# Kernel tuning notes

Measured on AMD Instinct MI355X. Metric: run time of the kernel, lower is better.

The kernel has to match this reference:

```python
import jax, jax.numpy as jnp
import numpy as np

B, T, IN, H, L, P = 512, 512, 1, 100, 4, 0.5  # batch, seq, input, hidden, layers, dropout


def setup_inputs() -> dict:
    key = jax.random.key(0)
    ks = jax.random.split(key, 12)
    k = 1.0 / np.sqrt(H)  # torch nn.LSTM init scale
    u = lambda kk, shape: jax.random.uniform(kk, shape, jnp.float32, -k, k)
    inp = {
        "x": jax.random.normal(ks[0], (B, T, IN), jnp.float32),
        "W_ih0": u(ks[1], (4 * H, IN)),          # layer 0 input weights
        "W_ih_rest": u(ks[2], (L - 1, 4 * H, H)),  # layers 1..3 input weights
        "W_hh": u(ks[3], (L, 4 * H, H)),
        "b_ih": u(ks[4], (L, 4 * H)),
        "b_hh": u(ks[5], (L, 4 * H)),
        "W_out": u(ks[6], (1, H)),
        "b_out": u(ks[7], (1,)),
        # inter-layer dropout keep-masks (torch applies dropout to outputs of layers 0..L-2)
        "drop_masks": jax.random.bernoulli(ks[8], 1.0 - P, (L - 1, B, T, H)).astype(jnp.float32),
    }
    return inp


def _lstm_layer(seq, Wih, Whh, b):
    # seq: [T, B, in_dim]; returns [T, B, H]. PyTorch gate order: i, f, g, o.
    h0 = jnp.zeros((seq.shape[1], Whh.shape[-1]), seq.dtype)

    def step(carry, xt):
        h, c = carry
        gates = xt @ Wih.T + h @ Whh.T + b  # [B, 4H]
        i, f, g, o = jnp.split(gates, 4, axis=-1)
        c = jax.nn.sigmoid(f) * c + jax.nn.sigmoid(i) * jnp.tanh(g)
        h = jax.nn.sigmoid(o) * jnp.tanh(c)
        return (h, c), h

    _, hs = jax.lax.scan(step, (h0, h0), seq)
    return hs


def reference(x, W_ih0, W_ih_rest, W_hh, b_ih, b_hh, W_out, b_out, drop_masks):
    scale = 1.0 / (1.0 - P)
    seq = jnp.swapaxes(x, 0, 1)  # [T, B, IN] (batch_first -> time-major)
    seq = _lstm_layer(seq, W_ih0, W_hh[0], b_ih[0] + b_hh[0])
    for l in range(1, L):
        seq = seq * (jnp.swapaxes(drop_masks[l - 1], 0, 1) * scale)
        seq = _lstm_layer(seq, W_ih_rest[l - 1], W_hh[l], b_ih[l] + b_hh[l])
    last = seq[-1]  # [B, H] == lstm_out[:, -1]
    return last @ W_out.T + b_out  # [B, 1]
```

## Files before the change

kernel.cpp:

```cpp
#include <hip/hip_runtime.h>
#include <cstdint>
#include <cstddef>

#define BB 512
#define TT 512
#define HH 100
#define G4 400

template<bool IS_L0, bool WRITE_DROP>
__global__ __launch_bounds__(448, 1)
void rec_kernel(const float* __restrict__ x,
                const float* __restrict__ xc,
                const float* __restrict__ Whh_l,
                const float* __restrict__ Wih0,
                const float* __restrict__ bih_l,
                const float* __restrict__ bhh_l,
                const float* __restrict__ dmask_l,
                float* __restrict__ hdrop,
                float* __restrict__ st_h,
                float* __restrict__ st_c)
{
    __shared__ float sh[G4 * HH];

    const int tid  = threadIdx.x;
    const int e    = (tid < 224) ? 0 : 1;
    const int off  = tid - e * 224;
    const int j    = off >> 1;
    const int role = off & 1;
    const bool active = (j < HH);
    const int jc   = active ? j : (HH - 1);
    const int r0   = role * 100 + jc;
    const int r1   = r0 + 200;
    const int b    = blockIdx.x * 2 + e;

    {
        const float4* src = (const float4*)Whh_l;
        float4* dst = (float4*)sh;
        for (int i = tid; i < G4 * HH / 4; i += 448) dst[i] = src[i];
    }
    __syncthreads();

    float4 wf0[25], wf1[25];
    {
        const float4* s0 = (const float4*)&sh[r0 * HH];
        const float4* s1 = (const float4*)&sh[r1 * HH];
        #pragma unroll
        for (int m = 0; m < 25; ++m) { wf0[m] = s0[m]; wf1[m] = s1[m]; }
    }
    __syncthreads();

    for (int i = tid; i < G4 * HH; i += 448) sh[i] = 0.f;

    float wx0 = 0.f, wx1 = 0.f, bs0 = 0.f, bs1 = 0.f;
    if (IS_L0) {
        wx0 = Wih0[r0];  bs0 = bih_l[r0] + bhh_l[r0];
        wx1 = Wih0[r1];  bs1 = bih_l[r1] + bhh_l[r1];
    }

    const bool isB = (role == 1);
    float c2 = 0.f, hlast = 0.f;

    __syncthreads();

    float gin0 = 0.f, gin1 = 0.f, xv = 0.f, mk = 0.f;
    if (IS_L0) {
        xv = x[(size_t)b * TT];
    } else {
        gin0 = xc[(size_t)b * G4 + r0];
        gin1 = xc[(size_t)b * G4 + r1];
    }
    if (WRITE_DROP && isB && active) mk = dmask_l[(size_t)b * TT * HH + jc];

    int cur = 0;
    for (int t = 0; t < TT; ++t) {
        const int tn = (t + 1 < TT) ? (t + 1) : t;

        float nxv = 0.f, ngin0 = 0.f, ngin1 = 0.f, nmk = 0.f;
        if (IS_L0) {
            nxv = x[(size_t)b * TT + tn];
        } else {
            const size_t base = (size_t)tn * (BB * G4) + (size_t)b * G4;
            ngin0 = xc[base + r0];
            ngin1 = xc[base + r1];
        }
        if (WRITE_DROP && isB && active)
            nmk = dmask_l[((size_t)b * TT + tn) * HH + jc];

        if (IS_L0) {
            gin0 = fmaf(xv, wx0, bs0);
            gin1 = fmaf(xv, wx1, bs1);
        }

        float a0 = 0.f, a0b = 0.f, a1 = 0.f, a1b = 0.f;
        {
            const float4* hp = (const float4*)&sh[cur * 224 + e * 112];
            #pragma unroll
            for (int m = 0; m < 25; ++m) {
                const float4 hv = hp[m];
                a0  = fmaf(wf0[m].x, hv.x, a0);
                a0b = fmaf(wf0[m].y, hv.y, a0b);
                a0  = fmaf(wf0[m].z, hv.z, a0);
                a0b = fmaf(wf0[m].w, hv.w, a0b);
                a1  = fmaf(wf1[m].x, hv.x, a1);
                a1b = fmaf(wf1[m].y, hv.y, a1b);
                a1  = fmaf(wf1[m].z, hv.z, a1);
                a1b = fmaf(wf1[m].w, hv.w, a1b);
            }
        }
        const float pre0 = a0 + a0b + gin0;
        const float pre1 = a1 + a1b + gin1;

        const float s0 = 1.f / (1.f + __expf(-pre0));
        const float E1 = __expf(isB ? (-pre1) : (pre1 + pre1));
        const float rr = 1.f / (1.f + E1);
        const float s1 = isB ? rr : fmaf(-2.f, rr, 1.f);

        const float pv   = s0 * s1;
        const float recv = __shfl_xor(pv, 1);

        const int nxt = cur ^ 1;
        if (isB) {
            c2 = fmaf(s0, c2, recv);
            const float Ec = __expf(c2 + c2);
            const float th = 1.f - 2.f / (Ec + 1.f);
            const float h  = s1 * th;
            hlast = h;
            if (active) {
                sh[nxt * 224 + e * 112 + j] = h;
                if (WRITE_DROP)
                    hdrop[((size_t)t * BB + b) * HH + j] = h * mk * 2.f;
            }
        }
        __syncthreads();
        cur = nxt;
        gin0 = ngin0; gin1 = ngin1; xv = nxv; mk = nmk;
    }

    if (isB && active) {
        st_h[(size_t)b * HH + j] = hlast;
        st_c[(size_t)b * HH + j] = c2;
    }
}

__global__ __launch_bounds__(256, 2)
void xc_gemm(const float* __restrict__ A,
             const float* __restrict__ W,
             const float* __restrict__ bih_l,
             const float* __restrict__ bhh_l,
             float* __restrict__ xc)
{
    __shared__ float At[HH][132];
    __shared__ float Bt[HH][68];

    const int tid = threadIdx.x;
    const int n0  = blockIdx.x * 64;
    const size_t m0 = (size_t)blockIdx.y * 128;

    for (int s = tid; s < 128 * 25; s += 256) {
        const int r = s / 25, kq = s - r * 25;
        const float4 v = *(const float4*)&A[(m0 + r) * HH + kq * 4];
        At[kq * 4 + 0][r] = v.x; At[kq * 4 + 1][r] = v.y;
        At[kq * 4 + 2][r] = v.z; At[kq * 4 + 3][r] = v.w;
    }
    for (int s = tid; s < 64 * 25; s += 256) {
        const int r = s / 25, kq = s - r * 25;
        const int col = n0 + r;
        float4 v = {0.f, 0.f, 0.f, 0.f};
        if (col < G4) v = *(const float4*)&W[(size_t)col * HH + kq * 4];
        Bt[kq * 4 + 0][r] = v.x; Bt[kq * 4 + 1][r] = v.y;
        Bt[kq * 4 + 2][r] = v.z; Bt[kq * 4 + 3][r] = v.w;
    }
    __syncthreads();

    const int tx = tid & 15;
    const int ty = tid >> 4;
    float acc[8][4];
    #pragma unroll
    for (int i = 0; i < 8; ++i)
        #pragma unroll
        for (int j = 0; j < 4; ++j) acc[i][j] = 0.f;

    #pragma unroll 4
    for (int k = 0; k < HH; ++k) {
        const float4 a0 = *(const float4*)&At[k][ty * 8];
        const float4 a1 = *(const float4*)&At[k][ty * 8 + 4];
        const float4 bv = *(const float4*)&Bt[k][tx * 4];
        const float av[8] = {a0.x, a0.y, a0.z, a0.w, a1.x, a1.y, a1.z, a1.w};
        #pragma unroll
        for (int i = 0; i < 8; ++i) {
            acc[i][0] = fmaf(av[i], bv.x, acc[i][0]);
            acc[i][1] = fmaf(av[i], bv.y, acc[i][1]);
            acc[i][2] = fmaf(av[i], bv.z, acc[i][2]);
            acc[i][3] = fmaf(av[i], bv.w, acc[i][3]);
        }
    }

    const int col = n0 + tx * 4;
    if (col < G4) {
        const float4 u = *(const float4*)&bih_l[col];
        const float4 v = *(const float4*)&bhh_l[col];
        const float4 bias = {u.x + v.x, u.y + v.y, u.z + v.z, u.w + v.w};
        #pragma unroll
        for (int i = 0; i < 8; ++i) {
            const size_t r = m0 + ty * 8 + i;
            float4 o = {acc[i][0] + bias.x, acc[i][1] + bias.y,
                        acc[i][2] + bias.z, acc[i][3] + bias.w};
            *(float4*)&xc[r * G4 + col] = o;
        }
    }
}

__global__ __launch_bounds__(256)
void out_kernel(const float* __restrict__ st_h3,
                const float* __restrict__ Wout,
                const float* __restrict__ bout,
                float* __restrict__ out)
{
    const int b = blockIdx.x * 256 + threadIdx.x;
    if (b < BB) {
        float sum = bout[0];
        #pragma unroll 4
        for (int k = 0; k < HH; ++k)
            sum = fmaf(st_h3[(size_t)b * HH + k], Wout[k], sum);
        out[b] = sum;
    }
}

extern "C" void kernel_launch(void* const* d_in, const int* in_sizes, int n_in,
                              void* d_out, int out_size, void* d_ws, size_t ws_size,
                              hipStream_t stream)
{
    const float* x     = (const float*)d_in[0];
    const float* Wih0  = (const float*)d_in[1];
    const float* WihR  = (const float*)d_in[2];
    const float* Whh   = (const float*)d_in[3];
    const float* bih   = (const float*)d_in[4];
    const float* bhh   = (const float*)d_in[5];
    const float* Wout  = (const float*)d_in[6];
    const float* bout  = (const float*)d_in[7];
    const float* dmask = (const float*)d_in[8];
    float* out = (float*)d_out;

    float* ws    = (float*)d_ws;
    float* xcb   = ws;
    float* hdrop = xcb + (size_t)TT * BB * G4;
    float* sth   = hdrop + (size_t)TT * BB * HH;
    float* stc   = sth + (size_t)4 * BB * HH;

    const dim3 rgrid(BB / 2), rblk(448);
    const dim3 ggrid(7, (TT * BB) / 128), gblk(256);

    rec_kernel<true, true><<<rgrid, rblk, 0, stream>>>(
        x, nullptr, Whh, Wih0, bih, bhh, dmask,
        hdrop, sth, stc);
    for (int l = 1; l < 4; ++l) {
        xc_gemm<<<ggrid, gblk, 0, stream>>>(
            hdrop, WihR + (size_t)(l - 1) * G4 * HH,
            bih + l * G4, bhh + l * G4, xcb);
        if (l < 3) {
            rec_kernel<false, true><<<rgrid, rblk, 0, stream>>>(
                nullptr, xcb, Whh + (size_t)l * G4 * HH,
                nullptr, nullptr, nullptr,
                dmask + (size_t)l * BB * TT * HH,
                hdrop, sth + (size_t)l * BB * HH, stc + (size_t)l * BB * HH);
        } else {
            rec_kernel<false, false><<<rgrid, rblk, 0, stream>>>(
                nullptr, xcb, Whh + (size_t)l * G4 * HH,
                nullptr, nullptr, nullptr,
                nullptr,
                nullptr, sth + (size_t)l * BB * HH, stc + (size_t)l * BB * HH);
        }
    }
    out_kernel<<<dim3(2), dim3(256), 0, stream>>>(sth + (size_t)3 * BB * HH, Wout, bout, out);
}
```

Baseline: 3.578 ms.

## Use split-bf16 MFMA for the layer input-projection GEMM

Replaces the FP32 FMA tiled GEMM that computes per-layer input projections with a matrix-core kernel. Each FP32 operand is split into high and low bf16 halves and four bf16 MFMAs approximate FP32 accuracy. A prep kernel pre-splits and pads the input weights once per call into workspace. It adds conversion work on the activation tile and a small extra launch. The recurrent kernel, which likely dominates runtime, is unchanged.

```diff
diff --git a/kernel.cpp b/kernel.cpp
--- a/kernel.cpp
+++ b/kernel.cpp
@@ -6,6 +6,17 @@
 #define TT 512
 #define HH 100
 #define G4 400
+
+typedef __attribute__((ext_vector_type(8))) short bf16x8;
+typedef __attribute__((ext_vector_type(4))) float f32x4;
+
+static __device__ inline void bsplit(float x, short& h, short& l) {
+    const unsigned u = __float_as_uint(x);
+    h = (short)(u >> 16);
+    const float fh = __uint_as_float(u & 0xffff0000u);
+    const float r  = x - fh;
+    l = (short)(__float_as_uint(r) >> 16);
+}
 
 template<bool IS_L0, bool WRITE_DROP>
 __global__ __launch_bounds__(448, 1)
@@ -142,70 +153,96 @@
     }
 }
 
+__global__ __launch_bounds__(256)
+void wprep(const float* __restrict__ WihR, short* __restrict__ whi,
+           short* __restrict__ wlo)
+{
+    const int idx = blockIdx.x * 256 + threadIdx.x;
+    if (idx >= 3 * 448 * 128) return;
+    const int k = idx & 127;
+    const int n = (idx >> 7) % 448;
+    const int l = idx / (448 * 128);
+    short h = 0, lo = 0;
+    if (n < G4 && k < HH)
+        bsplit(WihR[(size_t)l * G4 * HH + (size_t)n * HH + k], h, lo);
+    whi[idx] = h;
+    wlo[idx] = lo;
+}
+
 __global__ __launch_bounds__(256, 2)
-void xc_gemm(const float* __restrict__ A,
-             const float* __restrict__ W,
-             const float* __restrict__ bih_l,
-             const float* __restrict__ bhh_l,
-             float* __restrict__ xc)
-{
-    __shared__ float At[HH][132];
-    __shared__ float Bt[HH][68];
+void xc_gemm_mfma(const float* __restrict__ A,
+                  const short* __restrict__ whi,
+                  const short* __restrict__ wlo,
+                  const float* __restrict__ bih_l,
+                  const float* __restrict__ bhh_l,
+                  float* __restrict__ xc)
+{
+    __shared__ short Ah[128][136];
+    __shared__ short Al[128][136];
 
     const int tid = threadIdx.x;
-    const int n0  = blockIdx.x * 64;
+    const int nb  = blockIdx.x;
     const size_t m0 = (size_t)blockIdx.y * 128;
 
-    for (int s = tid; s < 128 * 25; s += 256) {
-        const int r = s / 25, kq = s - r * 25;
-        const float4 v = *(const float4*)&A[(m0 + r) * HH + kq * 4];
-        At[kq * 4 + 0][r] = v.x; At[kq * 4 + 1][r] = v.y;
-        At[kq * 4 + 2][r] = v.z; At[kq * 4 + 3][r] = v.w;
-    }
-    for (int s = tid; s < 64 * 25; s += 256) {
-        const int r = s / 25, kq = s - r * 25;
-        const int col = n0 + r;
-        float4 v = {0.f, 0.f, 0.f, 0.f};
-        if (col < G4) v = *(const float4*)&W[(size_t)col * HH + kq * 4];
-        Bt[kq * 4 + 0][r] = v.x; Bt[kq * 4 + 1][r] = v.y;
-        Bt[kq * 4 + 2][r] = v.z; Bt[kq * 4 + 3][r] = v.w;
+    for (int idx = tid; idx < 128 * 128; idx += 256) {
+        const int r = idx >> 7, k = idx & 127;
+        short h = 0, l = 0;
+        if (k < HH) bsplit(A[(m0 + r) * HH + k], h, l);
+        Ah[r][k] = h;
+        Al[r][k] = l;
     }
     __syncthreads();
 
-    const int tx = tid & 15;
-    const int ty = tid >> 4;
-    float acc[8][4];
+    const int w  = tid >> 6;
+    const int ln = tid & 63;
+    const int lr = ln & 15;
+    const int lk = (ln >> 4) * 8;
+
+    f32x4 acc[2][4] = {};
+
     #pragma unroll
-    for (int i = 0; i < 8; ++i)
+    for (int kc = 0; kc < 4; ++kc) {
+        const int kb = kc * 32 + lk;
+        bf16x8 ah[2], al[2], bh[4], bl[4];
         #pragma unroll
-        for (int j = 0; j < 4; ++j) acc[i][j] = 0.f;
-
-    #pragma unroll 4
-    for (int k = 0; k < HH; ++k) {
-        const float4 a0 = *(const float4*)&At[k][ty * 8];
-        const float4 a1 = *(const float4*)&At[k][ty * 8 + 4];
-        const float4 bv = *(const float4*)&Bt[k][tx * 4];
-        const float av[8] = {a0.x, a0.y, a0.z, a0.w, a1.x, a1.y, a1.z, a1.w};
+        for (int mt = 0; mt < 2; ++mt) {
+            const int row = w * 32 + mt * 16 + lr;
+            ah[mt] = *(const bf16x8*)&Ah[row][kb];
+            al[mt] = *(const bf16x8*)&Al[row][kb];
+        }
         #pragma unroll
-        for (int i = 0; i < 8; ++i) {
-            acc[i][0] = fmaf(av[i], bv.x, acc[i][0]);
-            acc[i][1] = fmaf(av[i], bv.y, acc[i][1]);
-            acc[i][2] = fmaf(av[i], bv.z, acc[i][2]);
-            acc[i][3] = fmaf(av[i], bv.w, acc[i][3]);
-        }
-    }
-
-    const int col = n0 + tx * 4;
-    if (col < G4) {
-        const float4 u = *(const float4*)&bih_l[col];
-        const float4 v = *(const float4*)&bhh_l[col];
-        const float4 bias = {u.x + v.x, u.y + v.y, u.z + v.z, u.w + v.w};
+        for (int nt = 0; nt < 4; ++nt) {
+            const size_t col = (size_t)nb * 64 + nt * 16 + lr;
+            bh[nt] = *(const bf16x8*)&whi[col * 128 + kb];
+            bl[nt] = *(const bf16x8*)&wlo[col * 128 + kb];
+        }
         #pragma unroll
-        for (int i = 0; i < 8; ++i) {
-            const size_t r = m0 + ty * 8 + i;
-            float4 o = {acc[i][0] + bias.x, acc[i][1] + bias.y,
-                        acc[i][2] + bias.z, acc[i][3] + bias.w};
-            *(float4*)&xc[r * G4 + col] = o;
+        for (int mt = 0; mt < 2; ++mt)
+            #pragma unroll
+            for (int nt = 0; nt < 4; ++nt) {
+                acc[mt][nt] = __builtin_amdgcn_mfma_f32_16x16x32_bf16(
+                    ah[mt], bh[nt], acc[mt][nt], 0, 0, 0);
+                acc[mt][nt] = __builtin_amdgcn_mfma_f32_16x16x32_bf16(
+                    ah[mt], bl[nt], acc[mt][nt], 0, 0, 0);
+                acc[mt][nt] = __builtin_amdgcn_mfma_f32_16x16x32_bf16(
+                    al[mt], bh[nt], acc[mt][nt], 0, 0, 0);
+                acc[mt][nt] = __builtin_amdgcn_mfma_f32_16x16x32_bf16(
+                    al[mt], bl[nt], acc[mt][nt], 0, 0, 0);
+            }
+    }
+
+    #pragma unroll
+    for (int nt = 0; nt < 4; ++nt) {
+        const int col = nb * 64 + nt * 16 + lr;
+        if (col < G4) {
+            const float bias = bih_l[col] + bhh_l[col];
+            #pragma unroll
+            for (int mt = 0; mt < 2; ++mt) {
+                const size_t rowb = m0 + w * 32 + mt * 16 + (ln >> 4) * 4;
+                #pragma unroll
+                for (int r = 0; r < 4; ++r)
+                    xc[(rowb + r) * G4 + col] = acc[mt][nt][r] + bias;
+            }
         }
     }
 }
@@ -246,16 +283,21 @@
     float* hdrop = xcb + (size_t)TT * BB * G4;
     float* sth   = hdrop + (size_t)TT * BB * HH;
     float* stc   = sth + (size_t)4 * BB * HH;
+    short* whi   = (short*)(stc + (size_t)4 * BB * HH);
+    short* wlo   = whi + (size_t)3 * 448 * 128;
 
     const dim3 rgrid(BB / 2), rblk(448);
     const dim3 ggrid(7, (TT * BB) / 128), gblk(256);
+
+    wprep<<<dim3((3 * 448 * 128 + 255) / 256), dim3(256), 0, stream>>>(WihR, whi, wlo);
 
     rec_kernel<true, true><<<rgrid, rblk, 0, stream>>>(
         x, nullptr, Whh, Wih0, bih, bhh, dmask,
         hdrop, sth, stc);
     for (int l = 1; l < 4; ++l) {
-        xc_gemm<<<ggrid, gblk, 0, stream>>>(
-            hdrop, WihR + (size_t)(l - 1) * G4 * HH,
+        xc_gemm_mfma<<<ggrid, gblk, 0, stream>>>(
+            hdrop, whi + (size_t)(l - 1) * 448 * 128,
+            wlo + (size_t)(l - 1) * 448 * 128,
             bih + l * G4, bhh + l * G4, xcb);
         if (l < 3) {
             rec_kernel<false, true><<<rgrid, rblk, 0, stream>>>(
```

After: 4.838 ms. 1.35x slower.

## Rewrite LSTM recurrence with bf16 MFMA over 16-sample batch tiles

Applied to the files above, without the earlier changes.

The recurrent kernel changes from per-thread scalar fp32 dot products, with 2 batch samples per block, to MFMA 16x16x32 bf16 matrix multiplies over 16 samples per block. W_hh is converted to bf16 in LDS with gate-interleaved columns so that one lane quad holds the i/f/g/o gates of a hidden unit, combined through shuffles. The hidden state is kept in LDS as bf16. This cuts the grid from 256 blocks to 32, reusing the weights across more samples but leaving most CUs idle. It also adds bf16 rounding error to the recurrent matmul.

```diff
diff --git a/kernel.cpp b/kernel.cpp
--- a/kernel.cpp
+++ b/kernel.cpp
@@ -7,138 +7,197 @@
 #define HH 100
 #define G4 400
 
+typedef __attribute__((ext_vector_type(8))) short bf16x8;
+typedef __attribute__((ext_vector_type(4))) float f32x4;
+
+static __device__ inline short tobf(float v) {
+    const unsigned u = __float_as_uint(v);
+    return (short)((u + 0x7fffu + ((u >> 16) & 1u)) >> 16);
+}
+
 template<bool IS_L0, bool WRITE_DROP>
-__global__ __launch_bounds__(448, 1)
-void rec_kernel(const float* __restrict__ x,
-                const float* __restrict__ xc,
-                const float* __restrict__ Whh_l,
-                const float* __restrict__ Wih0,
-                const float* __restrict__ bih_l,
-                const float* __restrict__ bhh_l,
-                const float* __restrict__ dmask_l,
-                float* __restrict__ hdrop,
-                float* __restrict__ st_h,
-                float* __restrict__ st_c)
+__global__ __launch_bounds__(512, 1)
+void rec_mfma(const float* __restrict__ x,
+              const float* __restrict__ xc,
+              const float* __restrict__ Whh_l,
+              const float* __restrict__ Wih0,
+              const float* __restrict__ bih_l,
+              const float* __restrict__ bhh_l,
+              const float* __restrict__ dmask_l,
+              float* __restrict__ hdrop,
+              float* __restrict__ st_h)
 {
-    __shared__ float sh[G4 * HH];
-
-    const int tid  = threadIdx.x;
-    const int e    = (tid < 224) ? 0 : 1;
-    const int off  = tid - e * 224;
-    const int j    = off >> 1;
-    const int role = off & 1;
-    const bool active = (j < HH);
-    const int jc   = active ? j : (HH - 1);
-    const int r0   = role * 100 + jc;
-    const int r1   = r0 + 200;
-    const int b    = blockIdx.x * 2 + e;
-
-    {
-        const float4* src = (const float4*)Whh_l;
-        float4* dst = (float4*)sh;
-        for (int i = tid; i < G4 * HH / 4; i += 448) dst[i] = src[i];
+    __shared__ short lds[400 * 136];
+
+    const int tid = threadIdx.x;
+    const int wv  = tid >> 6;
+    const int ln  = tid & 63;
+    const int lr  = ln & 15;
+    const int lk  = ln >> 4;
+    const int g   = ln & 3;
+    const bool isf = (g == 1);
+    const bool isg = (g == 2);
+    const int b0  = blockIdx.x * 16;
+
+    for (int i = tid; i < 400 * 136; i += 512) {
+        const int c = i / 136, k = i - c * 136;
+        short v = 0;
+        if (k < HH) {
+            const int u = c >> 2, gg = c & 3;
+            v = tobf(Whh_l[(size_t)(gg * HH + u) * HH + k]);
+        }
+        lds[i] = v;
     }
     __syncthreads();
 
-    float4 wf0[25], wf1[25];
-    {
-        const float4* s0 = (const float4*)&sh[r0 * HH];
-        const float4* s1 = (const float4*)&sh[r1 * HH];
-        #pragma unroll
-        for (int m = 0; m < 25; ++m) { wf0[m] = s0[m]; wf1[m] = s1[m]; }
+    bf16x8 wf[4][4];
+    #pragma unroll
+    for (int ti = 0; ti < 4; ++ti) {
+        const int tl = wv + ti * 8;
+        if (tl < 25) {
+            const int col = tl * 16 + lr;
+            #pragma unroll
+            for (int kc = 0; kc < 4; ++kc)
+                wf[ti][kc] = *(const bf16x8*)&lds[col * 136 + kc * 32 + lk * 8];
+        }
     }
     __syncthreads();
 
-    for (int i = tid; i < G4 * HH; i += 448) sh[i] = 0.f;
-
-    float wx0 = 0.f, wx1 = 0.f, bs0 = 0.f, bs1 = 0.f;
+    for (int i = tid; i < 400 * 136; i += 512) lds[i] = 0;
+
+    int rph[4], uu[4];
+    float wxv[4], bsv[4];
+    #pragma unroll
+    for (int ti = 0; ti < 4; ++ti) {
+        const int tl = wv + ti * 8;
+        if (tl < 25) {
+            const int col = tl * 16 + lr;
+            rph[ti] = (col & 3) * HH + (col >> 2);
+            uu[ti]  = col >> 2;
+            if (IS_L0) {
+                wxv[ti] = Wih0[rph[ti]];
+                bsv[ti] = bih_l[rph[ti]] + bhh_l[rph[ti]];
+            }
+        }
+    }
+
+    float c2[4][4];
+    #pragma unroll
+    for (int ti = 0; ti < 4; ++ti)
+        #pragma unroll
+        for (int r = 0; r < 4; ++r) c2[ti][r] = 0.f;
+
+    __syncthreads();
+
+    float ginc[4][4], xcur[4];
     if (IS_L0) {
-        wx0 = Wih0[r0];  bs0 = bih_l[r0] + bhh_l[r0];
-        wx1 = Wih0[r1];  bs1 = bih_l[r1] + bhh_l[r1];
-    }
-
-    const bool isB = (role == 1);
-    float c2 = 0.f, hlast = 0.f;
-
-    __syncthreads();
-
-    float gin0 = 0.f, gin1 = 0.f, xv = 0.f, mk = 0.f;
-    if (IS_L0) {
-        xv = x[(size_t)b * TT];
+        #pragma unroll
+        for (int r = 0; r < 4; ++r) xcur[r] = x[(size_t)(b0 + lk * 4 + r) * TT];
     } else {
-        gin0 = xc[(size_t)b * G4 + r0];
-        gin1 = xc[(size_t)b * G4 + r1];
-    }
-    if (WRITE_DROP && isB && active) mk = dmask_l[(size_t)b * TT * HH + jc];
+        #pragma unroll
+        for (int ti = 0; ti < 4; ++ti) {
+            const int tl = wv + ti * 8;
+            if (tl < 25) {
+                #pragma unroll
+                for (int r = 0; r < 4; ++r)
+                    ginc[ti][r] = xc[(size_t)(b0 + lk * 4 + r) * G4 + rph[ti]];
+            }
+        }
+    }
 
     int cur = 0;
     for (int t = 0; t < TT; ++t) {
         const int tn = (t + 1 < TT) ? (t + 1) : t;
 
-        float nxv = 0.f, ngin0 = 0.f, ngin1 = 0.f, nmk = 0.f;
+        float ginn[4][4], xnxt[4];
         if (IS_L0) {
-            nxv = x[(size_t)b * TT + tn];
+            #pragma unroll
+            for (int r = 0; r < 4; ++r)
+                xnxt[r] = x[(size_t)(b0 + lk * 4 + r) * TT + tn];
         } else {
-            const size_t base = (size_t)tn * (BB * G4) + (size_t)b * G4;
-            ngin0 = xc[base + r0];
-            ngin1 = xc[base + r1];
-        }
-        if (WRITE_DROP && isB && active)
-            nmk = dmask_l[((size_t)b * TT + tn) * HH + jc];
-
-        if (IS_L0) {
-            gin0 = fmaf(xv, wx0, bs0);
-            gin1 = fmaf(xv, wx1, bs1);
-        }
-
-        float a0 = 0.f, a0b = 0.f, a1 = 0.f, a1b = 0.f;
-        {
-            const float4* hp = (const float4*)&sh[cur * 224 + e * 112];
-            #pragma unroll
-            for (int m = 0; m < 25; ++m) {
-                const float4 hv = hp[m];
-                a0  = fmaf(wf0[m].x, hv.x, a0);
-                a0b = fmaf(wf0[m].y, hv.y, a0b);
-                a0  = fmaf(wf0[m].z, hv.z, a0);
-                a0b = fmaf(wf0[m].w, hv.w, a0b);
-                a1  = fmaf(wf1[m].x, hv.x, a1);
-                a1b = fmaf(wf1[m].y, hv.y, a1b);
-                a1  = fmaf(wf1[m].z, hv.z, a1);
-                a1b = fmaf(wf1[m].w, hv.w, a1b);
-            }
-        }
-        const float pre0 = a0 + a0b + gin0;
-        const float pre1 = a1 + a1b + gin1;
-
-        const float s0 = 1.f / (1.f + __expf(-pre0));
-        const float E1 = __expf(isB ? (-pre1) : (pre1 + pre1));
-        const float rr = 1.f / (1.f + E1);
-        const float s1 = isB ? rr : fmaf(-2.f, rr, 1.f);
-
-        const float pv   = s0 * s1;
-        const float recv = __shfl_xor(pv, 1);
+            const size_t base = (size_t)tn * BB * G4;
+            #pragma unroll
+            for (int ti = 0; ti < 4; ++ti) {
+                const int tl = wv + ti * 8;
+                if (tl < 25) {
+                    #pragma unroll
+                    for (int r = 0; r < 4; ++r)
+                        ginn[ti][r] = xc[base + (size_t)(b0 + lk * 4 + r) * G4 + rph[ti]];
+                }
+            }
+        }
+        float mk[4][4];
+        if (WRITE_DROP && isf) {
+            #pragma unroll
+            for (int ti = 0; ti < 4; ++ti) {
+                const int tl = wv + ti * 8;
+                if (tl < 25) {
+                    #pragma unroll
+                    for (int r = 0; r < 4; ++r)
+                        mk[ti][r] = dmask_l[(size_t)(b0 + lk * 4 + r) * TT * HH
+                                            + (size_t)t * HH + uu[ti]];
+                }
+            }
+        }
+
+        bf16x8 af[4];
+        #pragma unroll
+        for (int kc = 0; kc < 4; ++kc)
+            af[kc] = *(const bf16x8*)&lds[cur * 2176 + lr * 136 + kc * 32 + lk * 8];
 
         const int nxt = cur ^ 1;
-        if (isB) {
-            c2 = fmaf(s0, c2, recv);
-            const float Ec = __expf(c2 + c2);
-            const float th = 1.f - 2.f / (Ec + 1.f);
-            const float h  = s1 * th;
-            hlast = h;
-            if (active) {
-                sh[nxt * 224 + e * 112 + j] = h;
-                if (WRITE_DROP)
-                    hdrop[((size_t)t * BB + b) * HH + j] = h * mk * 2.f;
+        #pragma unroll
+        for (int ti = 0; ti < 4; ++ti) {
+            const int tl = wv + ti * 8;
+            if (tl < 25) {
+                f32x4 acc;
+                if (IS_L0) {
+                    #pragma unroll
+                    for (int r = 0; r < 4; ++r)
+                        acc[r] = fmaf(xcur[r], wxv[ti], bsv[ti]);
+                } else {
+                    #pragma unroll
+                    for (int r = 0; r < 4; ++r) acc[r] = ginc[ti][r];
+                }
+                #pragma unroll
+                for (int kc = 0; kc < 4; ++kc)
+                    acc = __builtin_amdgcn_mfma_f32_16x16x32_bf16(
+                        af[kc], wf[ti][kc], acc, 0, 0, 0);
+
+                #pragma unroll
+                for (int r = 0; r < 4; ++r) {
+                    const float pre = acc[r];
+                    const float E  = __expf(isg ? (pre + pre) : (-pre));
+                    const float rr = 1.f / (1.f + E);
+                    const float a  = isg ? fmaf(-2.f, rr, 1.f) : rr;
+                    const float t2 = __shfl_xor(a, 2);
+                    const float pr = a * t2;
+                    const float t1 = __shfl_xor(pr, 1);
+                    if (isf) {
+                        const float c = fmaf(a, c2[ti][r], t1);
+                        c2[ti][r] = c;
+                        const float Ec = __expf(c + c);
+                        const float th = 1.f - 2.f / (Ec + 1.f);
+                        const float h  = t2 * th;
+                        const int  e   = lk * 4 + r;
+                        lds[nxt * 2176 + e * 136 + uu[ti]] = tobf(h);
+                        if (WRITE_DROP)
+                            hdrop[((size_t)t * BB + b0 + e) * HH + uu[ti]] =
+                                h * mk[ti][r] * 2.f;
+                        if (t == TT - 1 && st_h)
+                            st_h[(size_t)(b0 + e) * HH + uu[ti]] = h;
+                    }
+                }
             }
         }
         __syncthreads();
         cur = nxt;
-        gin0 = ngin0; gin1 = ngin1; xv = nxv; mk = nmk;
-    }
-
-    if (isB && active) {
-        st_h[(size_t)b * HH + j] = hlast;
-        st_c[(size_t)b * HH + j] = c2;
+        #pragma unroll
+        for (int ti = 0; ti < 4; ++ti)
+            #pragma unroll
+            for (int r = 0; r < 4; ++r) ginc[ti][r] = ginn[ti][r];
+        #pragma unroll
+        for (int r = 0; r < 4; ++r) xcur[r] = xnxt[r];
     }
 }
 
@@ -178,7 +237,7 @@
     #pragma unroll
     for (int i = 0; i < 8; ++i)
         #pragma unroll
-        for (int j = 0; j < 4; ++j) acc[i][j] = 0.f;
+        for (int jj = 0; jj < 4; ++jj) acc[i][jj] = 0.f;
 
     #pragma unroll 4
     for (int k = 0; k < HH; ++k) {
@@ -245,31 +304,30 @@
     float* xcb   = ws;
     float* hdrop = xcb + (size_t)TT * BB * G4;
     float* sth   = hdrop + (size_t)TT * BB * HH;
-    float* stc   = sth + (size_t)4 * BB * HH;
-
-    const dim3 rgrid(BB / 2), rblk(448);
+
+    const dim3 rgrid(BB / 16), rblk(512);
     const dim3 ggrid(7, (TT * BB) / 128), gblk(256);
 
-    rec_kernel<true, true><<<rgrid, rblk, 0, stream>>>(
+    rec_mfma<true, true><<<rgrid, rblk, 0, stream>>>(
         x, nullptr, Whh, Wih0, bih, bhh, dmask,
-        hdrop, sth, stc);
+        hdrop, nullptr);
     for (int l = 1; l < 4; ++l) {
         xc_gemm<<<ggrid, gblk, 0, stream>>>(
             hdrop, WihR + (size_t)(l - 1) * G4 * HH,
             bih + l * G4, bhh + l * G4, xcb);
         if (l < 3) {
-            rec_kernel<false, true><<<rgrid, rblk, 0, stream>>>(
+            rec_mfma<false, true><<<rgrid, rblk, 0, stream>>>(
                 nullptr, xcb, Whh + (size_t)l * G4 * HH,
                 nullptr, nullptr, nullptr,
                 dmask + (size_t)l * BB * TT * HH,
-                hdrop, sth + (size_t)l * BB * HH, stc + (size_t)l * BB * HH);
+                hdrop, nullptr);
         } else {
-            rec_kernel<false, false><<<rgrid, rblk, 0, stream>>>(
+            rec_mfma<false, false><<<rgrid, rblk, 0, stream>>>(
                 nullptr, xcb, Whh + (size_t)l * G4 * HH,
                 nullptr, nullptr, nullptr,
                 nullptr,
-                nullptr, sth + (size_t)l * BB * HH, stc + (size_t)l * BB * HH);
-        }
-    }
-    out_kernel<<<dim3(2), dim3(256), 0, stream>>>(sth + (size_t)3 * BB * HH, Wout, bout, out);
-}
+                nullptr, sth);
+        }
+    }
+    out_kernel<<<dim3(2), dim3(256), 0, stream>>>(sth, Wout, bout, out);
+}
```

Measured after the change: 10.06 ms. 2.81x slower.
